# Optimization experiments

Measured on AMD Instinct MI355X. Metric: run time of the kernel, lower is better.

Reference implementation:

```python
import jax, jax.numpy as jnp
import numpy as np
from jax import lax

EPS_LN = 1e-5
EPS_BN = 1e-5

def layernorm(x, g, b):
    m = x.mean(-1, keepdims=True)
    v = x.var(-1, keepdims=True)
    return (x - m) / jnp.sqrt(v + EPS_LN) * g + b

def conv(x, w, b):
    y = lax.conv_general_dilated(x, w, (1, 1), 'SAME', dimension_numbers=('NCHW', 'OIHW', 'NCHW'))
    return y + b[None, :, None, None]

def bnorm(x, g, b, m, v):
    # BatchNorm2d in eval mode (running stats)
    return (x - m[None, :, None, None]) / jnp.sqrt(v[None, :, None, None] + EPS_BN) * g[None, :, None, None] + b[None, :, None, None]

def maxpool2(x):
    return lax.reduce_window(x, -jnp.inf, lax.max, (1, 1, 2, 2), (1, 1, 2, 2), 'VALID')

def l2norm_rows(x):
    n = jnp.linalg.norm(x, axis=1, keepdims=True)
    return x / jnp.maximum(n, 1e-12)

def fastslow(x, sw, sb, fw, fb, lng, lnb, lr, decay):
    # one hebbian fast-weight update step (torch does this in no_grad on x.detach())
    xs = lax.stop_gradient(x)
    fw = fw * decay
    fb = fb * decay
    slow_out = xs @ sw.T + sb
    xn = l2norm_rows(xs)
    son = l2norm_rows(slow_out)
    hebb = son.T @ xn / xs.shape[0]          # [out,in] outer-product update
    fw = fw + lr * hebb
    wn = jnp.linalg.norm(fw, axis=1, keepdims=True)
    fw = jnp.where(wn > 0.25, fw * (0.25 / (wn + 1e-8)), fw)
    fb = jnp.clip(fb + lr * son.mean(0), -0.2, 0.2)
    fw = lax.stop_gradient(fw)
    fb = lax.stop_gradient(fb)
    out = x @ (sw + fw).T + (sb + fb)
    return layernorm(out, lng, lnb)

def forward(x, c1_w, c1_b, bn1_g, bn1_b, bn1_m, bn1_v,
            c2_w, c2_b, bn2_g, bn2_b, bn2_m, bn2_v,
            c3_w, c3_b, bn3_g, bn3_b, bn3_m, bn3_v,
            core_w, core_b, core_lng, core_lnb,
            fp_sw, fp_sb, fp_fw, fp_fb, fp_lng, fp_lnb,
            sp_sw, sp_sb, sp_fw, sp_fb, sp_lng, sp_lnb,
            int_w, int_b, int_lng, int_lnb, mem,
            cn_w1, cn_b1, cn_lng, cn_lnb, cn_w2, cn_b2,
            pr_w, pr_b, pr_lng, pr_lnb, cl_w, cl_b):
    # encoder (dropout layers are identity in eval)
    h = jax.nn.relu(bnorm(conv(x, c1_w, c1_b), bn1_g, bn1_b, bn1_m, bn1_v)); h = maxpool2(h)
    h = jax.nn.relu(bnorm(conv(h, c2_w, c2_b), bn2_g, bn2_b, bn2_m, bn2_v)); h = maxpool2(h)
    h = jax.nn.relu(bnorm(conv(h, c3_w, c3_b), bn3_g, bn3_b, bn3_m, bn3_v))
    h = h.mean((2, 3))  # AdaptiveAvgPool2d((1,1)) + Flatten -> [B,256]
    # core
    hc = jax.nn.relu(layernorm(h @ core_w.T + core_b, core_lng, core_lnb))
    # dual system: memory EMA (no_grad), fast/slow hebbian paths, integrator
    mem_new = lax.stop_gradient(0.9 * mem + 0.1 * hc.mean(0, keepdims=True))
    fast_out = fastslow(hc, fp_sw, fp_sb, fp_fw, fp_fb, fp_lng, fp_lnb, 0.015, 0.95)
    slow_out = fastslow(hc + 0.3 * mem_new, sp_sw, sp_sb, sp_fw, sp_fb, sp_lng, sp_lnb, 0.005, 0.97)
    comb = jnp.concatenate([fast_out, slow_out], axis=1)
    hd = layernorm(comb @ int_w.T + int_b, int_lng, int_lnb)
    hd = hd + hc  # residual
    # consciousness: phi from eigen-entropy of feature covariance (no_grad)
    a = lax.stop_gradient(hd)
    am = a.mean(0, keepdims=True)
    ast = jnp.std(a, axis=0, keepdims=True, ddof=1) + 1e-6
    an = (a - am) / ast
    n = a.shape[0]
    cov = an.T @ an / (n - 1) + 1e-4 * jnp.eye(a.shape[1], dtype=a.dtype)
    eigs = jnp.clip(jnp.linalg.eigvalsh(cov), 0.0, None)
    en = eigs / (eigs.sum() + 1e-8)
    entropy = -(en * jnp.log(en + 1e-8)).sum()
    phi = entropy / jnp.log(jnp.asarray(float(a.shape[1]), a.dtype))
    phi_eff = jnp.clip(0.3 * phi, 0.0, 1.0)  # running_phi starts at 0: 0.7*0 + 0.3*phi
    net = jax.nn.relu(layernorm(hd @ cn_w1.T + cn_b1, cn_lng, cn_lnb)) @ cn_w2.T + cn_b2
    strength = jax.nn.sigmoid((phi_eff - 0.1) * 5.0)
    coef = jnp.where(phi_eff > 0.1, strength, 0.1)
    hcon = hd + coef * net
    # projection + classifier
    hp = jax.nn.relu(layernorm(hcon @ pr_w.T + pr_b, pr_lng, pr_lnb))
    return hp @ cl_w.T + cl_b

def setup_inputs() -> dict:
    key = jax.random.key(0)
    ks = iter(jax.random.split(key, 64))
    def nrm(shape, s=0.05):
        return jax.random.normal(next(ks), shape, jnp.float32) * s
    B, D = 512, 256
    d = {}
    d['x'] = jax.random.normal(next(ks), (B, 3, 32, 32), jnp.float32)
    for i, (co, ci) in enumerate([(64, 3), (128, 64), (256, 128)], 1):
        d[f'c{i}_w'] = nrm((co, ci, 3, 3))
        d[f'c{i}_b'] = jnp.zeros((co,), jnp.float32)
        d[f'bn{i}_g'] = jnp.ones((co,), jnp.float32)
        d[f'bn{i}_b'] = jnp.zeros((co,), jnp.float32)
        d[f'bn{i}_m'] = jnp.zeros((co,), jnp.float32)
        d[f'bn{i}_v'] = jnp.ones((co,), jnp.float32)
    d['core_w'] = nrm((D, D)); d['core_b'] = jnp.zeros((D,), jnp.float32)
    d['core_lng'] = jnp.ones((D,), jnp.float32); d['core_lnb'] = jnp.zeros((D,), jnp.float32)
    for p in ['fp', 'sp']:
        d[f'{p}_sw'] = nrm((D, D)); d[f'{p}_sb'] = jnp.zeros((D,), jnp.float32)
        d[f'{p}_fw'] = nrm((D, D), 0.01); d[f'{p}_fb'] = jnp.zeros((D,), jnp.float32)
        d[f'{p}_lng'] = jnp.ones((D,), jnp.float32); d[f'{p}_lnb'] = jnp.zeros((D,), jnp.float32)
    d['int_w'] = nrm((D, 2 * D)); d['int_b'] = jnp.zeros((D,), jnp.float32)
    d['int_lng'] = jnp.ones((D,), jnp.float32); d['int_lnb'] = jnp.zeros((D,), jnp.float32)
    d['mem'] = jnp.zeros((1, D), jnp.float32)
    d['cn_w1'] = nrm((D, D)); d['cn_b1'] = jnp.zeros((D,), jnp.float32)
    d['cn_lng'] = jnp.ones((D,), jnp.float32); d['cn_lnb'] = jnp.zeros((D,), jnp.float32)
    d['cn_w2'] = nrm((D, D)); d['cn_b2'] = jnp.zeros((D,), jnp.float32)
    d['pr_w'] = nrm((128, D)); d['pr_b'] = jnp.zeros((128,), jnp.float32)
    d['pr_lng'] = jnp.ones((128,), jnp.float32); d['pr_lnb'] = jnp.zeros((128,), jnp.float32)
    d['cl_w'] = nrm((10, 128)); d['cl_b'] = jnp.zeros((10,), jnp.float32)
    return d

def reference(x, c1_w, c1_b, bn1_g, bn1_b, bn1_m, bn1_v,
              c2_w, c2_b, bn2_g, bn2_b, bn2_m, bn2_v,
              c3_w, c3_b, bn3_g, bn3_b, bn3_m, bn3_v,
              core_w, core_b, core_lng, core_lnb,
              fp_sw, fp_sb, fp_fw, fp_fb, fp_lng, fp_lnb,
              sp_sw, sp_sb, sp_fw, sp_fb, sp_lng, sp_lnb,
              int_w, int_b, int_lng, int_lnb, mem,
              cn_w1, cn_b1, cn_lng, cn_lnb, cn_w2, cn_b2,
              pr_w, pr_b, pr_lng, pr_lnb, cl_w, cl_b):
    return forward(x, c1_w, c1_b, bn1_g, bn1_b, bn1_m, bn1_v,
                   c2_w, c2_b, bn2_g, bn2_b, bn2_m, bn2_v,
                   c3_w, c3_b, bn3_g, bn3_b, bn3_m, bn3_v,
                   core_w, core_b, core_lng, core_lnb,
                   fp_sw, fp_sb, fp_fw, fp_fb, fp_lng, fp_lnb,
                   sp_sw, sp_sb, sp_fw, sp_fb, sp_lng, sp_lnb,
                   int_w, int_b, int_lng, int_lnb, mem,
                   cn_w1, cn_b1, cn_lng, cn_lnb, cn_w2, cn_b2,
                   pr_w, pr_b, pr_lng, pr_lnb, cl_w, cl_b)
```

## Files before the change

### kernel.cpp

```cpp
#include <hip/hip_runtime.h>
#include <hip/hip_bf16.h>

template<int NT>
__device__ __forceinline__ float block_sum(float v, float* red, int t) {
  red[t] = v; __syncthreads();
#pragma unroll
  for (int s = NT/2; s > 0; s >>= 1) {
    if (t < s) red[t] += red[t+s];
    __syncthreads();
  }
  float r = red[0];
  __syncthreads();
  return r;
}

template<int DIN>
__device__ __forceinline__ float dot_f32_row(const float* __restrict__ wr, const float* __restrict__ xs) {
  float acc = 0.f;
  const float4* wp = reinterpret_cast<const float4*>(wr);
#pragma unroll 4
  for (int i = 0; i < DIN/4; ++i) {
    float4 w4 = wp[i];
    acc += w4.x*xs[i*4] + w4.y*xs[i*4+1] + w4.z*xs[i*4+2] + w4.w*xs[i*4+3];
  }
  return acc;
}

__global__ __launch_bounds__(256) void k_conv1(const float* __restrict__ x, const float* __restrict__ w1,
    const float* __restrict__ cb, const float* __restrict__ g, const float* __restrict__ bb,
    const float* __restrict__ m, const float* __restrict__ v, float* __restrict__ p1)
{
  __shared__ float xs[3][34][34];
  __shared__ float ws1[64*27];
  __shared__ float A1[64], B1[64];
  int b = blockIdx.x, t = threadIdx.x;
  float* xsf = &xs[0][0][0];
  for (int i = t; i < 3*34*34; i += 256) xsf[i] = 0.f;
  for (int i = t; i < 64*27; i += 256) ws1[i] = w1[i];
  if (t < 64) {
    float sc = g[t] * rsqrtf(v[t] + 1e-5f);
    A1[t] = sc;
    B1[t] = (cb[t] - m[t])*sc + bb[t];
  }
  __syncthreads();
  for (int i = t; i < 3*1024; i += 256) {
    int ci = i >> 10, rem = i & 1023, y = rem >> 5, xx = rem & 31;
    xs[ci][y+1][xx+1] = x[((size_t)b*3 + ci)*1024 + rem];
  }
  __syncthreads();
  int py = t >> 4, px = t & 15;
  int y0 = py*2, x0 = px*2;
  for (int co = 0; co < 64; ++co) {
    float a00=0.f,a01=0.f,a10=0.f,a11=0.f;
#pragma unroll
    for (int ci = 0; ci < 3; ++ci) {
      const float* xb = &xs[ci][y0][x0];
      float r0a=xb[0],r0b=xb[1],r0c=xb[2],r0d=xb[3];
      float r1a=xb[34],r1b=xb[35],r1c=xb[36],r1d=xb[37];
      float r2a=xb[68],r2b=xb[69],r2c=xb[70],r2d=xb[71];
      float r3a=xb[102],r3b=xb[103],r3c=xb[104],r3d=xb[105];
      const float* wp = &ws1[co*27 + ci*9];
      float ww0=wp[0],ww1=wp[1],ww2=wp[2],ww3=wp[3],ww4=wp[4],ww5=wp[5],ww6=wp[6],ww7=wp[7],ww8=wp[8];
      a00 += ww0*r0a+ww1*r0b+ww2*r0c + ww3*r1a+ww4*r1b+ww5*r1c + ww6*r2a+ww7*r2b+ww8*r2c;
      a01 += ww0*r0b+ww1*r0c+ww2*r0d + ww3*r1b+ww4*r1c+ww5*r1d + ww6*r2b+ww7*r2c+ww8*r2d;
      a10 += ww0*r1a+ww1*r1b+ww2*r1c + ww3*r2a+ww4*r2b+ww5*r2c + ww6*r3a+ww7*r3b+ww8*r3c;
      a11 += ww0*r1b+ww1*r1c+ww2*r1d + ww3*r2b+ww4*r2c+ww5*r2d + ww6*r3b+ww7*r3c+ww8*r3d;
    }
    float sc = A1[co], sh = B1[co];
    float vmax = fmaxf(fmaxf(a00*sc+sh, a01*sc+sh), fmaxf(a10*sc+sh, a11*sc+sh));
    vmax = fmaxf(vmax, 0.f);
    p1[(((size_t)b*64 + co)*16 + py)*16 + px] = vmax;
  }
}

__global__ __launch_bounds__(256) void k_conv2(const float* __restrict__ p1, const float* __restrict__ w2,
    const float* __restrict__ cb, const float* __restrict__ g, const float* __restrict__ bb,
    const float* __restrict__ m, const float* __restrict__ v, float* __restrict__ p2)
{
  __shared__ float xs[64][18][18];
  __shared__ float wchT[576*5];
  __shared__ float A2[128], B2[128];
  int b = blockIdx.x, t = threadIdx.x;
  float* xsf = &xs[0][0][0];
  for (int i = t; i < 64*18*18; i += 256) xsf[i] = 0.f;
  if (t < 128) {
    float sc = g[t] * rsqrtf(v[t] + 1e-5f);
    A2[t] = sc;
    B2[t] = (cb[t] - m[t])*sc + bb[t];
  }
  __syncthreads();
  for (int i = t; i < 64*256; i += 256) {
    int ci = i >> 8, rem = i & 255, y = rem >> 4, xx = rem & 15;
    xs[ci][y+1][xx+1] = p1[((size_t)b*64 + ci)*256 + rem];
  }
  int lane = t & 3, pos = t >> 2;
  int py = pos >> 3, px = pos & 7;
  int y0 = py*2, x0 = px*2;
  for (int it = 0; it < 32; ++it) {
    __syncthreads();
    for (int i = t; i < 2304; i += 256) {
      int rem = i % 576, co = i / 576;
      wchT[rem*5 + co] = w2[(size_t)it*2304 + i];
    }
    __syncthreads();
    float a00=0.f,a01=0.f,a10=0.f,a11=0.f;
    for (int ci = 0; ci < 64; ++ci) {
      const float* xb = &xs[ci][y0][x0];
      float r0a=xb[0],r0b=xb[1],r0c=xb[2],r0d=xb[3];
      float r1a=xb[18],r1b=xb[19],r1c=xb[20],r1d=xb[21];
      float r2a=xb[36],r2b=xb[37],r2c=xb[38],r2d=xb[39];
      float r3a=xb[54],r3b=xb[55],r3c=xb[56],r3d=xb[57];
      const float* wp = &wchT[(ci*9)*5 + lane];
      float ww0=wp[0],ww1=wp[5],ww2=wp[10],ww3=wp[15],ww4=wp[20],ww5=wp[25],ww6=wp[30],ww7=wp[35],ww8=wp[40];
      a00 += ww0*r0a+ww1*r0b+ww2*r0c + ww3*r1a+ww4*r1b+ww5*r1c + ww6*r2a+ww7*r2b+ww8*r2c;
      a01 += ww0*r0b+ww1*r0c+ww2*r0d + ww3*r1b+ww4*r1c+ww5*r1d + ww6*r2b+ww7*r2c+ww8*r2d;
      a10 += ww0*r1a+ww1*r1b+ww2*r1c + ww3*r2a+ww4*r2b+ww5*r2c + ww6*r3a+ww7*r3b+ww8*r3c;
      a11 += ww0*r1b+ww1*r1c+ww2*r1d + ww3*r2b+ww4*r2c+ww5*r2d + ww6*r3b+ww7*r3c+ww8*r3d;
    }
    int co = it*4 + lane;
    float sc = A2[co], sh = B2[co];
    float vmax = fmaxf(fmaxf(a00*sc+sh, a01*sc+sh), fmaxf(a10*sc+sh, a11*sc+sh));
    vmax = fmaxf(vmax, 0.f);
    p2[(((size_t)b*128 + co)*8 + py)*8 + px] = vmax;
  }
}

__global__ __launch_bounds__(256) void k_conv3(const float* __restrict__ p2, const float* __restrict__ w3,
    const float* __restrict__ cb, const float* __restrict__ g, const float* __restrict__ bb,
    const float* __restrict__ m, const float* __restrict__ v, float* __restrict__ h)
{
  __shared__ float xs[128][10][10];
  __shared__ float wchT[1152*17];
  __shared__ float A3[256], B3[256];
  __shared__ float red2[256];
  int b = blockIdx.x, t = threadIdx.x;
  float* xsf = &xs[0][0][0];
  for (int i = t; i < 128*100; i += 256) xsf[i] = 0.f;
  {
    float sc = g[t] * rsqrtf(v[t] + 1e-5f);
    A3[t] = sc;
    B3[t] = (cb[t] - m[t])*sc + bb[t];
  }
  __syncthreads();
  for (int i = t; i < 128*64; i += 256) {
    int ci = i >> 6, rem = i & 63, y = rem >> 3, xx = rem & 7;
    xs[ci][y+1][xx+1] = p2[((size_t)b*128 + ci)*64 + rem];
  }
  int lane = t & 15, cluster = t >> 4;
  int cy = cluster >> 2, cx = cluster & 3;
  int y0 = cy*2, x0 = cx*2;
  for (int it = 0; it < 16; ++it) {
    __syncthreads();
    for (int i = t; i < 18432; i += 256) {
      int rem = i % 1152, co = i / 1152;
      wchT[rem*17 + co] = w3[(size_t)it*18432 + i];
    }
    __syncthreads();
    float a00=0.f,a01=0.f,a10=0.f,a11=0.f;
    for (int ci = 0; ci < 128; ++ci) {
      const float* xb = &xs[ci][y0][x0];
      float r0a=xb[0],r0b=xb[1],r0c=xb[2],r0d=xb[3];
      float r1a=xb[10],r1b=xb[11],r1c=xb[12],r1d=xb[13];
      float r2a=xb[20],r2b=xb[21],r2c=xb[22],r2d=xb[23];
      float r3a=xb[30],r3b=xb[31],r3c=xb[32],r3d=xb[33];
      const float* wp = &wchT[(ci*9)*17 + lane];
      float ww0=wp[0],ww1=wp[17],ww2=wp[34],ww3=wp[51],ww4=wp[68],ww5=wp[85],ww6=wp[102],ww7=wp[119],ww8=wp[136];
      a00 += ww0*r0a+ww1*r0b+ww2*r0c + ww3*r1a+ww4*r1b+ww5*r1c + ww6*r2a+ww7*r2b+ww8*r2c;
      a01 += ww0*r0b+ww1*r0c+ww2*r0d + ww3*r1b+ww4*r1c+ww5*r1d + ww6*r2b+ww7*r2c+ww8*r2d;
      a10 += ww0*r1a+ww1*r1b+ww2*r1c + ww3*r2a+ww4*r2b+ww5*r2c + ww6*r3a+ww7*r3b+ww8*r3c;
      a11 += ww0*r1b+ww1*r1c+ww2*r1d + ww3*r2b+ww4*r2c+ww5*r2d + ww6*r3b+ww7*r3c+ww8*r3d;
    }
    int co = it*16 + lane;
    float sc = A3[co], sh = B3[co];
    float local = fmaxf(a00*sc+sh,0.f)+fmaxf(a01*sc+sh,0.f)+fmaxf(a10*sc+sh,0.f)+fmaxf(a11*sc+sh,0.f);
    red2[cluster*16 + lane] = local;
    __syncthreads();
    if (t < 16) {
      float s2 = 0.f;
      for (int c2 = 0; c2 < 16; ++c2) s2 += red2[c2*16 + t];
      h[(size_t)b*256 + it*16 + t] = s2 * (1.f/64.f);
    }
  }
}

template<int DIN, int DOUT, bool RELU, bool RESID>
__global__ __launch_bounds__(DOUT) void k_lin_ln(
    const float* __restrict__ in, const float* __restrict__ W, const float* __restrict__ bias,
    const float* __restrict__ g, const float* __restrict__ be,
    const float* __restrict__ resid, float* __restrict__ out, int ostride, int ooff)
{
  __shared__ float xs[DIN];
  __shared__ float red[DOUT];
  int b = blockIdx.x, t = threadIdx.x;
  for (int i = t; i < DIN; i += DOUT) xs[i] = in[(size_t)b*DIN + i];
  __syncthreads();
  float acc = dot_f32_row<DIN>(W + (size_t)t*DIN, xs) + bias[t];
  float mean = block_sum<DOUT>(acc, red, t) * (1.f/DOUT);
  float dv = acc - mean;
  float var = block_sum<DOUT>(dv*dv, red, t) * (1.f/DOUT);
  float y = dv * rsqrtf(var + 1e-5f) * g[t] + be[t];
  if (RELU) y = fmaxf(y, 0.f);
  if (RESID) y += resid[(size_t)b*DOUT + t];
  out[(size_t)b*ostride + ooff + t] = y;
}

__global__ __launch_bounds__(256) void k_lin_rownorm(const float* __restrict__ in, const float* __restrict__ sw,
    const float* __restrict__ sb, float* __restrict__ sout, float* __restrict__ xninv, float* __restrict__ sninv)
{
  int b = blockIdx.x, t = threadIdx.x;
  __shared__ float xs[256];
  __shared__ float red[256];
  xs[t] = in[(size_t)b*256 + t];
  __syncthreads();
  float acc = dot_f32_row<256>(sw + (size_t)t*256, xs) + sb[t];
  sout[(size_t)b*256 + t] = acc;
  float xn2 = block_sum<256>(xs[t]*xs[t], red, t);
  float sn2 = block_sum<256>(acc*acc, red, t);
  if (t == 0) {
    xninv[b] = 1.f / fmaxf(sqrtf(xn2), 1e-12f);
    sninv[b] = 1.f / fmaxf(sqrtf(sn2), 1e-12f);
  }
}

__global__ __launch_bounds__(256) void k_hebb(const float* __restrict__ x, const float* __restrict__ s,
    const float* __restrict__ xninv, const float* __restrict__ sninv,
    const float* __restrict__ sw, const float* __restrict__ fw,
    const float* __restrict__ sb, const float* __restrict__ fb,
    float lr, float decay, float* __restrict__ weff, float* __restrict__ beff)
{
  int o = blockIdx.x, t = threadIdx.x;
  __shared__ float c[512];
  __shared__ float sonb[512];
  __shared__ float red[256];
  for (int b = t; b < 512; b += 256) {
    float son = s[(size_t)b*256 + o] * sninv[b];
    sonb[b] = son;
    c[b] = son * xninv[b];
  }
  __syncthreads();
  float acc = 0.f;
  for (int b = 0; b < 512; ++b) acc += c[b] * x[(size_t)b*256 + t];
  float hebb = acc * (1.f/512.f);
  float fwn = fw[(size_t)o*256 + t] * decay + lr * hebb;
  float wn2 = block_sum<256>(fwn*fwn, red, t);
  float wn = sqrtf(wn2);
  float scale = (wn > 0.25f) ? 0.25f/(wn + 1e-8f) : 1.f;
  weff[(size_t)o*256 + t] = sw[(size_t)o*256 + t] + fwn*scale;
  float sm = block_sum<256>(sonb[t] + sonb[t+256], red, t) * (1.f/512.f);
  if (t == 0) {
    float fbe = fb[o] * decay + lr * sm;
    fbe = fminf(fmaxf(fbe, -0.2f), 0.2f);
    beff[o] = sb[o] + fbe;
  }
}

__global__ __launch_bounds__(256) void k_mem(const float* __restrict__ hc, const float* __restrict__ mem,
                                             float* __restrict__ memnew)
{
  int t = threadIdx.x;
  float s = 0.f;
  for (int b = 0; b < 512; ++b) s += hc[(size_t)b*256 + t];
  memnew[t] = 0.9f*mem[t] + 0.1f*(s * (1.f/512.f));
}

__global__ __launch_bounds__(256) void k_x2(const float* __restrict__ hc, const float* __restrict__ memnew,
                                            float* __restrict__ x2)
{
  int i = blockIdx.x*256 + threadIdx.x;
  x2[i] = hc[i] + 0.3f*memnew[i & 255];
}

__global__ __launch_bounds__(256) void k_colstats(const float* __restrict__ hd, float* __restrict__ am,
                                                  float* __restrict__ ainv)
{
  int t = threadIdx.x;
  float s1 = 0.f;
  for (int b = 0; b < 512; ++b) s1 += hd[(size_t)b*256 + t];
  float mean = s1 * (1.f/512.f);
  float s2 = 0.f;
  for (int b = 0; b < 512; ++b) { float dv = hd[(size_t)b*256 + t] - mean; s2 += dv*dv; }
  am[t] = mean;
  ainv[t] = 1.f/(sqrtf(s2 * (1.f/511.f)) + 1e-6f);
}

__global__ __launch_bounds__(256) void k_cov(const float* __restrict__ hd, const float* __restrict__ am,
    const float* __restrict__ ainv, float* __restrict__ cov)
{
  int i = blockIdx.x, t = threadIdx.x;
  __shared__ float ci[512];
  float ami = am[i], aii = ainv[i];
  for (int b = t; b < 512; b += 256) ci[b] = (hd[(size_t)b*256 + i] - ami)*aii;
  __syncthreads();
  float amj = am[t], aij = ainv[t];
  float acc = 0.f;
  for (int b = 0; b < 512; ++b) acc += ci[b] * (hd[(size_t)b*256 + t] - amj);
  float cval = acc * aij * (1.f/511.f) + ((i == t) ? 1e-4f : 0.f);
  cov[(size_t)i*256 + t] = cval;
}

__global__ __launch_bounds__(1024) void k_tridiag(const float* __restrict__ A, float* __restrict__ d, float* __restrict__ e)
{
  const int n = 256;
  __shared__ float tri[32896];
  __shared__ float v[256], q[256];
  __shared__ float ppw[16][257];
  __shared__ float redA[4], red4[4];
  __shared__ float sH;
  int t = threadIdx.x;
  int wid = t >> 6, lane = t & 63;

  for (int i = t; i < 32896; i += 1024) {
    int r = (int)((sqrtf(8.f*(float)i + 1.f) - 1.f) * 0.5f);
    while ((r+1)*(r+2)/2 <= i) ++r;
    while (r*(r+1)/2 > i) --r;
    int c = i - r*(r+1)/2;
    tri[i] = A[(size_t)r*n + c];
  }
  __syncthreads();

  for (int k = 0; k < n-2; ++k) {
    int m = n-1-k;
    int base = k+1;

    float xi = 0.f;
    if (t < m) {
      int R = base + t;
      xi = tri[R*(R+1)/2 + k];
      v[t] = xi;
    }
    if (t < 256) {
      float val = xi*xi;
#pragma unroll
      for (int mk = 1; mk < 64; mk <<= 1) val += __shfl_xor(val, mk, 64);
      if (lane == 0) redA[wid] = val;
    }
    __syncthreads();
    if (t == 0) {
      float sigma = redA[0]+redA[1]+redA[2]+redA[3];
      float x0 = v[0];
      float alpha = (x0 >= 0.f) ? -sqrtf(sigma) : sqrtf(sigma);
      sH = sigma - x0*alpha;
      e[k] = alpha;
      v[0] = x0 - alpha;
    }
    __syncthreads();
    float H = sH;
    if (H <= 1e-32f) continue;

    float p0=0.f, p1=0.f, p2=0.f, p3=0.f;
    for (int r = wid; r < m; r += 16) {
      int R = base + r;
      int rowoff = R*(R+1)/2 + base;
      float vr = v[r];
      float dot = 0.f;
#pragma unroll
      for (int c = 0; c < 4; ++c) {
        if (64*c <= r) {
          int j = 64*c + lane;
          float val = (j <= r) ? tri[rowoff + j] : 0.f;
          dot += val * v[j];
          float sval = (j < r) ? val : 0.f;
          float contrib = sval * vr;
          if (c == 0) p0 += contrib; else if (c == 1) p1 += contrib;
          else if (c == 2) p2 += contrib; else p3 += contrib;
        }
      }
#pragma unroll
      for (int mk = 1; mk < 64; mk <<= 1) dot += __shfl_xor(dot, mk, 64);
      if (lane == (r & 63)) {
        int sl = r >> 6;
        if (sl == 0) p0 += dot; else if (sl == 1) p1 += dot;
        else if (sl == 2) p2 += dot; else p3 += dot;
      }
    }
    ppw[wid][lane]      = p0;
    ppw[wid][64+lane]   = p1;
    ppw[wid][128+lane]  = p2;
    ppw[wid][192+lane]  = p3;
    __syncthreads();

    float pt = 0.f;
    if (t < 256) {
      float kv = 0.f;
#pragma unroll
      for (int w2 = 0; w2 < 16; ++w2) pt += ppw[w2][t];
      pt /= H;
      if (t < m) kv = v[t] * pt;
#pragma unroll
      for (int mk = 1; mk < 64; mk <<= 1) kv += __shfl_xor(kv, mk, 64);
      if (lane == 0) red4[wid] = kv;
    }
    __syncthreads();
    if (t < m) {
      float Kv = (red4[0]+red4[1]+red4[2]+red4[3]) / (2.f*H);
      q[t] = pt - Kv*v[t];
    }
    __syncthreads();

    for (int r = wid; r < m; r += 16) {
      int R = base + r;
      int rowoff = R*(R+1)/2 + base;
      float vr = v[r], qr = q[r];
#pragma unroll
      for (int c = 0; c < 4; ++c) {
        if (64*c <= r) {
          int j = 64*c + lane;
          if (j <= r) tri[rowoff + j] -= vr*q[j] + qr*v[j];
        }
      }
    }
    __syncthreads();
  }
  if (t == 0) {
    e[n-2] = tri[((n-1)*n)/2 + (n-2)];
    e[n-1] = 0.f;
  }
  if (t < n) d[t] = tri[(t*(t+1))/2 + t];
}

__global__ __launch_bounds__(256) void k_eig_coef(const float* __restrict__ dg, const float* __restrict__ eg,
                                                  float* __restrict__ coefout)
{
  const int n = 256;
  int t = threadIdx.x;
  __shared__ float sd[256], se2[256], sea[256], red[256];
  sd[t] = dg[t];
  float ev = (t < n-1) ? eg[t] : 0.f;
  se2[t] = ev*ev;
  sea[t] = fabsf(ev);
  __syncthreads();
  float r = ((t > 0) ? sea[t-1] : 0.f) + sea[t];
  red[t] = sd[t] - r; __syncthreads();
  for (int s = 128; s > 0; s >>= 1) { if (t < s) red[t] = fminf(red[t], red[t+s]); __syncthreads(); }
  float glo = red[0] - 1e-3f; __syncthreads();
  red[t] = sd[t] + r; __syncthreads();
  for (int s = 128; s > 0; s >>= 1) { if (t < s) red[t] = fmaxf(red[t], red[t+s]); __syncthreads(); }
  float ghi = red[0] + 1e-3f; __syncthreads();

  float lo = glo, hi = ghi;
  for (int it = 0; it < 40; ++it) {
    float mid = 0.5f*(lo + hi);
    int cnt = 0;
    float qq = sd[0] - mid;
    cnt += (qq < 0.f);
    for (int i = 1; i < n; ++i) {
      float denom = qq;
      if (fabsf(denom) < 1e-20f) denom = (denom < 0.f) ? -1e-20f : 1e-20f;
      qq = sd[i] - mid - se2[i-1]/denom;
      cnt += (qq < 0.f);
    }
    if (cnt <= t) lo = mid; else hi = mid;
  }
  float lam = fmaxf(0.5f*(lo + hi), 0.f);
  float tot = block_sum<256>(lam, red, t) + 1e-8f;
  float en = lam / tot;
  float contrib = -en * logf(en + 1e-8f);
  float ent = block_sum<256>(contrib, red, t);
  if (t == 0) {
    float phi = ent / logf(256.f);
    float phi_eff = fminf(fmaxf(0.3f*phi, 0.f), 1.f);
    float strength = 1.f/(1.f + expf(-(phi_eff - 0.1f)*5.f));
    coefout[0] = (phi_eff > 0.1f) ? strength : 0.1f;
  }
}

__global__ __launch_bounds__(256) void k_cn2(const float* __restrict__ t1, const float* __restrict__ W,
    const float* __restrict__ bias, const float* __restrict__ hd, const float* __restrict__ coefp,
    float* __restrict__ hcon)
{
  __shared__ float xs[256];
  int b = blockIdx.x, t = threadIdx.x;
  xs[t] = t1[(size_t)b*256 + t];
  __syncthreads();
  float acc = dot_f32_row<256>(W + (size_t)t*256, xs) + bias[t];
  hcon[(size_t)b*256 + t] = hd[(size_t)b*256 + t] + coefp[0]*acc;
}

__global__ __launch_bounds__(64) void k_cls(const float* __restrict__ hp, const float* __restrict__ W,
    const float* __restrict__ bias, float* __restrict__ out)
{
  int b = blockIdx.x, t = threadIdx.x;
  __shared__ float xs[128];
  if (t < 64) { xs[t] = hp[(size_t)b*128 + t]; xs[t+64] = hp[(size_t)b*128 + t + 64]; }
  __syncthreads();
  if (t < 10) {
    float acc = bias[t];
    const float* wr = W + (size_t)t*128;
    for (int i = 0; i < 128; ++i) acc += wr[i]*xs[i];
    out[(size_t)b*10 + t] = acc;
  }
}

extern "C" void kernel_launch(void* const* d_in, const int* in_sizes, int n_in,
                              void* d_out, int out_size, void* d_ws, size_t ws_size,
                              hipStream_t stream)
{
  (void)in_sizes; (void)n_in; (void)out_size; (void)ws_size;
  const float* x     = (const float*)d_in[0];
  const float* c1w   = (const float*)d_in[1];
  const float* c1b   = (const float*)d_in[2];
  const float* bn1g  = (const float*)d_in[3];
  const float* bn1b  = (const float*)d_in[4];
  const float* bn1m  = (const float*)d_in[5];
  const float* bn1v  = (const float*)d_in[6];
  const float* c2w   = (const float*)d_in[7];
  const float* c2b   = (const float*)d_in[8];
  const float* bn2g  = (const float*)d_in[9];
  const float* bn2b  = (const float*)d_in[10];
  const float* bn2m  = (const float*)d_in[11];
  const float* bn2v  = (const float*)d_in[12];
  const float* c3w   = (const float*)d_in[13];
  const float* c3b   = (const float*)d_in[14];
  const float* bn3g  = (const float*)d_in[15];
  const float* bn3b  = (const float*)d_in[16];
  const float* bn3m  = (const float*)d_in[17];
  const float* bn3v  = (const float*)d_in[18];
  const float* corew = (const float*)d_in[19];
  const float* coreb = (const float*)d_in[20];
  const float* corelng = (const float*)d_in[21];
  const float* corelnb = (const float*)d_in[22];
  const float* fpsw  = (const float*)d_in[23];
  const float* fpsb  = (const float*)d_in[24];
  const float* fpfw  = (const float*)d_in[25];
  const float* fpfb  = (const float*)d_in[26];
  const float* fplng = (const float*)d_in[27];
  const float* fplnb = (const float*)d_in[28];
  const float* spsw  = (const float*)d_in[29];
  const float* spsb  = (const float*)d_in[30];
  const float* spfw  = (const float*)d_in[31];
  const float* spfb  = (const float*)d_in[32];
  const float* splng = (const float*)d_in[33];
  const float* splnb = (const float*)d_in[34];
  const float* intw  = (const float*)d_in[35];
  const float* intb  = (const float*)d_in[36];
  const float* intlng= (const float*)d_in[37];
  const float* intlnb= (const float*)d_in[38];
  const float* memi  = (const float*)d_in[39];
  const float* cnw1  = (const float*)d_in[40];
  const float* cnb1  = (const float*)d_in[41];
  const float* cnlng = (const float*)d_in[42];
  const float* cnlnb = (const float*)d_in[43];
  const float* cnw2  = (const float*)d_in[44];
  const float* cnb2  = (const float*)d_in[45];
  const float* prw   = (const float*)d_in[46];
  const float* prb   = (const float*)d_in[47];
  const float* prlng = (const float*)d_in[48];
  const float* prlnb = (const float*)d_in[49];
  const float* clw   = (const float*)d_in[50];
  const float* clb   = (const float*)d_in[51];
  float* out = (float*)d_out;

  float* w = (float*)d_ws;
  size_t off = 0;
  auto alloc = [&](size_t nel) { float* p = w + off; off += nel; return p; };
  float* p1     = alloc((size_t)512*64*16*16);
  float* p2     = alloc((size_t)512*128*8*8);
  float* h      = alloc(512*256);
  float* hc     = alloc(512*256);
  float* x2     = alloc(512*256);
  float* s      = alloc(512*256);
  float* xninv  = alloc(512);
  float* sninv  = alloc(512);
  float* memnew = alloc(256);
  float* weff   = alloc(256*256);
  float* beff   = alloc(256);
  float* comb   = alloc((size_t)512*512);
  float* hd     = alloc(512*256);
  float* am     = alloc(256);
  float* ainv   = alloc(256);
  float* cov    = alloc(256*256);
  float* dvec   = alloc(256);
  float* evec   = alloc(256);
  float* coefb  = alloc(8);
  float* t1     = alloc(512*256);
  float* hcon   = alloc(512*256);
  float* hp     = alloc(512*128);

  k_conv1<<<512,256,0,stream>>>(x, c1w, c1b, bn1g, bn1b, bn1m, bn1v, p1);
  k_conv2<<<512,256,0,stream>>>(p1, c2w, c2b, bn2g, bn2b, bn2m, bn2v, p2);
  k_conv3<<<512,256,0,stream>>>(p2, c3w, c3b, bn3g, bn3b, bn3m, bn3v, h);
  k_lin_ln<256,256,true,false><<<512,256,0,stream>>>(h, corew, coreb, corelng, corelnb, nullptr, hc, 256, 0);
  k_mem<<<1,256,0,stream>>>(hc, memi, memnew);
  k_x2<<<512,256,0,stream>>>(hc, memnew, x2);
  k_lin_rownorm<<<512,256,0,stream>>>(hc, fpsw, fpsb, s, xninv, sninv);
  k_hebb<<<256,256,0,stream>>>(hc, s, xninv, sninv, fpsw, fpfw, fpsb, fpfb, 0.015f, 0.95f, weff, beff);
  k_lin_ln<256,256,false,false><<<512,256,0,stream>>>(hc, weff, beff, fplng, fplnb, nullptr, comb, 512, 0);
  k_lin_rownorm<<<512,256,0,stream>>>(x2, spsw, spsb, s, xninv, sninv);
  k_hebb<<<256,256,0,stream>>>(x2, s, xninv, sninv, spsw, spfw, spsb, spfb, 0.005f, 0.97f, weff, beff);
  k_lin_ln<256,256,false,false><<<512,256,0,stream>>>(x2, weff, beff, splng, splnb, nullptr, comb, 512, 256);
  k_lin_ln<512,256,false,true><<<512,256,0,stream>>>(comb, intw, intb, intlng, intlnb, hc, hd, 256, 0);
  k_colstats<<<1,256,0,stream>>>(hd, am, ainv);
  k_cov<<<256,256,0,stream>>>(hd, am, ainv, cov);
  k_tridiag<<<1,1024,0,stream>>>(cov, dvec, evec);
  k_eig_coef<<<1,256,0,stream>>>(dvec, evec, coefb);
  k_lin_ln<256,256,true,false><<<512,256,0,stream>>>(hd, cnw1, cnb1, cnlng, cnlnb, nullptr, t1, 256, 0);
  k_cn2<<<512,256,0,stream>>>(t1, cnw2, cnb2, hd, coefb, hcon);
  k_lin_ln<256,128,true,false><<<512,128,0,stream>>>(hcon, prw, prb, prlng, prlnb, nullptr, hp, 128, 0);
  k_cls<<<512,64,0,stream>>>(hp, clw, clb, out);
}
```

Before: 4.172 ms.

## Fuse tail linear layers, trim tridiag inner loops, cut bisection iterations

Merges the connector linear+LN+ReLU with its second linear, and the projector linear+LN+ReLU with the classifier, so the intermediates stay in shared memory. This removes two launches and two global round-trips. The Householder tridiagonalisation loops now split into full 64-wide chunks plus one masked tail, which drops the per-chunk predicates. Eigenvalue bisection drops from 40 to 28 iterations, which lowers precision of the eigenvalues used for the entropy coefficient.

```diff
diff --git a/kernel.cpp b/kernel.cpp
--- a/kernel.cpp
+++ b/kernel.cpp
@@ -353,16 +353,29 @@
       int rowoff = R*(R+1)/2 + base;
       float vr = v[r];
       float dot = 0.f;
-#pragma unroll
-      for (int c = 0; c < 4; ++c) {
-        if (64*c <= r) {
-          int j = 64*c + lane;
-          float val = (j <= r) ? tri[rowoff + j] : 0.f;
-          dot += val * v[j];
-          float sval = (j < r) ? val : 0.f;
-          float contrib = sval * vr;
-          if (c == 0) p0 += contrib; else if (c == 1) p1 += contrib;
-          else if (c == 2) p2 += contrib; else p3 += contrib;
+      int nf = r >> 6;
+      for (int c = 0; c < nf; ++c) {
+        int j = (c << 6) + lane;
+        float val = tri[rowoff + j];
+        dot = fmaf(val, v[j], dot);
+        float contrib = val * vr;
+        if (c == 0) p0 += contrib;
+        else if (c == 1) p1 += contrib;
+        else if (c == 2) p2 += contrib;
+        else p3 += contrib;
+      }
+      {
+        int j = (nf << 6) + lane;
+        if (j <= r) {
+          float val = tri[rowoff + j];
+          dot = fmaf(val, v[j], dot);
+          if (j < r) {
+            float contrib = val * vr;
+            if (nf == 0) p0 += contrib;
+            else if (nf == 1) p1 += contrib;
+            else if (nf == 2) p2 += contrib;
+            else p3 += contrib;
+          }
         }
       }
 #pragma unroll
@@ -401,13 +414,13 @@
       int R = base + r;
       int rowoff = R*(R+1)/2 + base;
       float vr = v[r], qr = q[r];
-#pragma unroll
-      for (int c = 0; c < 4; ++c) {
-        if (64*c <= r) {
-          int j = 64*c + lane;
-          if (j <= r) tri[rowoff + j] -= vr*q[j] + qr*v[j];
-        }
+      int nfd = (r + 1) >> 6;
+      for (int c = 0; c < nfd; ++c) {
+        int j = (c << 6) + lane;
+        tri[rowoff + j] -= fmaf(vr, q[j], qr*v[j]);
       }
+      int j = (nfd << 6) + lane;
+      if (j <= r) tri[rowoff + j] -= fmaf(vr, q[j], qr*v[j]);
     }
     __syncthreads();
   }
@@ -438,7 +451,7 @@
   float ghi = red[0] + 1e-3f; __syncthreads();
 
   float lo = glo, hi = ghi;
-  for (int it = 0; it < 40; ++it) {
+  for (int it = 0; it < 28; ++it) {
     float mid = 0.5f*(lo + hi);
     int cnt = 0;
     float qq = sd[0] - mid;
@@ -464,30 +477,49 @@
   }
 }
 
-__global__ __launch_bounds__(256) void k_cn2(const float* __restrict__ t1, const float* __restrict__ W,
-    const float* __restrict__ bias, const float* __restrict__ hd, const float* __restrict__ coefp,
+__global__ __launch_bounds__(256) void k_cn(const float* __restrict__ hd, const float* __restrict__ W1,
+    const float* __restrict__ b1, const float* __restrict__ g, const float* __restrict__ be,
+    const float* __restrict__ W2, const float* __restrict__ b2, const float* __restrict__ coefp,
     float* __restrict__ hcon)
 {
   __shared__ float xs[256];
+  __shared__ float t1s[256];
+  __shared__ float red[256];
   int b = blockIdx.x, t = threadIdx.x;
-  xs[t] = t1[(size_t)b*256 + t];
+  xs[t] = hd[(size_t)b*256 + t];
+  __syncthreads();
+  float acc = dot_f32_row<256>(W1 + (size_t)t*256, xs) + b1[t];
+  float mean = block_sum<256>(acc, red, t) * (1.f/256.f);
+  float dv = acc - mean;
+  float var = block_sum<256>(dv*dv, red, t) * (1.f/256.f);
+  t1s[t] = fmaxf(dv * rsqrtf(var + 1e-5f) * g[t] + be[t], 0.f);
+  __syncthreads();
+  float acc2 = dot_f32_row<256>(W2 + (size_t)t*256, t1s) + b2[t];
+  hcon[(size_t)b*256 + t] = xs[t] + coefp[0]*acc2;
+}
+
+__global__ __launch_bounds__(128) void k_pr_cls(const float* __restrict__ hcon, const float* __restrict__ W,
+    const float* __restrict__ bias, const float* __restrict__ g, const float* __restrict__ be,
+    const float* __restrict__ Wc, const float* __restrict__ bc, float* __restrict__ out)
+{
+  __shared__ float xs[256];
+  __shared__ float hp[128];
+  __shared__ float red[128];
+  int b = blockIdx.x, t = threadIdx.x;
+  xs[t] = hcon[(size_t)b*256 + t];
+  xs[t+128] = hcon[(size_t)b*256 + t + 128];
   __syncthreads();
   float acc = dot_f32_row<256>(W + (size_t)t*256, xs) + bias[t];
-  hcon[(size_t)b*256 + t] = hd[(size_t)b*256 + t] + coefp[0]*acc;
-}
-
-__global__ __launch_bounds__(64) void k_cls(const float* __restrict__ hp, const float* __restrict__ W,
-    const float* __restrict__ bias, float* __restrict__ out)
-{
-  int b = blockIdx.x, t = threadIdx.x;
-  __shared__ float xs[128];
-  if (t < 64) { xs[t] = hp[(size_t)b*128 + t]; xs[t+64] = hp[(size_t)b*128 + t + 64]; }
+  float mean = block_sum<128>(acc, red, t) * (1.f/128.f);
+  float dv = acc - mean;
+  float var = block_sum<128>(dv*dv, red, t) * (1.f/128.f);
+  hp[t] = fmaxf(dv * rsqrtf(var + 1e-5f) * g[t] + be[t], 0.f);
   __syncthreads();
   if (t < 10) {
-    float acc = bias[t];
-    const float* wr = W + (size_t)t*128;
-    for (int i = 0; i < 128; ++i) acc += wr[i]*xs[i];
-    out[(size_t)b*10 + t] = acc;
+    float a2 = bc[t];
+    const float* wr = Wc + (size_t)t*128;
+    for (int i = 0; i < 128; ++i) a2 += wr[i]*hp[i];
+    out[(size_t)b*10 + t] = a2;
   }
 }
 
@@ -572,9 +604,7 @@
   float* dvec   = alloc(256);
   float* evec   = alloc(256);
   float* coefb  = alloc(8);
-  float* t1     = alloc(512*256);
   float* hcon   = alloc(512*256);
-  float* hp     = alloc(512*128);
 
   k_conv1<<<512,256,0,stream>>>(x, c1w, c1b, bn1g, bn1b, bn1m, bn1v, p1);
   k_conv2<<<512,256,0,stream>>>(p1, c2w, c2b, bn2g, bn2b, bn2m, bn2v, p2);
@@ -593,8 +623,6 @@
   k_cov<<<256,256,0,stream>>>(hd, am, ainv, cov);
   k_tridiag<<<1,1024,0,stream>>>(cov, dvec, evec);
   k_eig_coef<<<1,256,0,stream>>>(dvec, evec, coefb);
-  k_lin_ln<256,256,true,false><<<512,256,0,stream>>>(hd, cnw1, cnb1, cnlng, cnlnb, nullptr, t1, 256, 0);
-  k_cn2<<<512,256,0,stream>>>(t1, cnw2, cnb2, hd, coefb, hcon);
-  k_lin_ln<256,128,true,false><<<512,128,0,stream>>>(hcon, prw, prb, prlng, prlnb, nullptr, hp, 128, 0);
-  k_cls<<<512,64,0,stream>>>(hp, clw, clb, out);
-}
+  k_cn<<<512,256,0,stream>>>(hd, cnw1, cnb1, cnlng, cnlnb, cnw2, cnb2, coefb, hcon);
+  k_pr_cls<<<512,128,0,stream>>>(hcon, prw, prb, prlng, prlnb, clw, clb, out);
+}
```

Result: slower. 4.618 ms (+10.7%).
